# Kernel optimization log

Hardware: AMD Instinct MI355X
Metric: run time of the kernel (lower is better)

The kernel has to match this reference:

```python
import jax, jax.numpy as jnp
import numpy as np

B, N, D = 4, 256, 128
HID = 128
IN_DIM = 4 * D + 4  # h_i, h_j, |h_i-h_j|, h_i*h_j + 2 base + 2 completion feats


def setup_inputs() -> dict:
    key = jax.random.key(0)
    k1, k2, k3, k4, k5, k6, k7 = jax.random.split(key, 7)
    node_latents = jax.random.normal(k1, (B, N, D), dtype=jnp.float32)
    base_edge_logits = jax.random.normal(k2, (B, N, N), dtype=jnp.float32)
    completion_logits = jax.random.normal(k3, (B, N, N), dtype=jnp.float32)
    # MLP params (build_mlp: Linear(in,hid) -> ReLU -> Linear(hid,1) for num_layers=2)
    s1 = 1.0 / np.sqrt(IN_DIM)
    s2 = 1.0 / np.sqrt(HID)
    W1 = jax.random.uniform(k4, (IN_DIM, HID), minval=-s1, maxval=s1, dtype=jnp.float32)
    b1 = jax.random.uniform(k5, (HID,), minval=-s1, maxval=s1, dtype=jnp.float32)
    W2 = jax.random.uniform(k6, (HID, 1), minval=-s2, maxval=s2, dtype=jnp.float32)
    b2 = jax.random.uniform(k7, (1,), minval=-s2, maxval=s2, dtype=jnp.float32)
    return {"node_latents": node_latents, "base_edge_logits": base_edge_logits,
            "completion_logits": completion_logits, "W1": W1, "b1": b1, "W2": W2, "b2": b2}


def reference(node_latents, base_edge_logits, completion_logits, W1, b1, W2, b2):
    bsz, num_nodes, hidden_dim = node_latents.shape
    h_i = jnp.broadcast_to(node_latents[:, :, None, :], (bsz, num_nodes, num_nodes, hidden_dim))
    h_j = jnp.broadcast_to(node_latents[:, None, :, :], (bsz, num_nodes, num_nodes, hidden_dim))
    base = jnp.clip(base_edge_logits, -20.0, 20.0)
    comp = jnp.clip(completion_logits, -20.0, 20.0)
    pair_feat = jnp.concatenate([
        h_i, h_j, jnp.abs(h_i - h_j), h_i * h_j,
        base[..., None], jax.nn.sigmoid(base)[..., None],
        comp[..., None], jax.nn.sigmoid(comp)[..., None],
    ], axis=-1)  # [B, N, N, IN_DIM]
    hdn = jax.nn.relu(jnp.einsum('bijf,fh->bijh', pair_feat, W1) + b1)
    logits = (jnp.einsum('bijh,ho->bijo', hdn, W2) + b2)[..., 0]  # [B, N, N]
    logits = 0.5 * (logits + jnp.swapaxes(logits, 1, 2))
    diag = jnp.eye(num_nodes, dtype=bool)[None]
    return jnp.where(diag, jnp.float32(-1e9), logits)
```

## Files before the change

kernel.cpp:

```cpp
#include <hip/hip_runtime.h>
#include <cstdint>


typedef float f32x4 __attribute__((ext_vector_type(4)));

#define INV256 0.00390625f

__device__ __forceinline__ uint32_t pk4(float a, float b, float c, float d) {
  uint32_t u = __builtin_amdgcn_cvt_pk_fp8_f32(a, b, 0, false);
  u = __builtin_amdgcn_cvt_pk_fp8_f32(c, d, u, true);
  return u;
}
__device__ __forceinline__ uint32_t pkbf2(float lo, float hi) {
  uint32_t l = __builtin_bit_cast(uint32_t, lo);
  uint32_t h = __builtin_bit_cast(uint32_t, hi);
  return (l >> 16) | (h & 0xffff0000u);
}
__device__ __forceinline__ float ulo(uint32_t u) {
  return __builtin_bit_cast(float, u << 16);
}
__device__ __forceinline__ float uhi(uint32_t u) {
  return __builtin_bit_cast(float, u & 0xffff0000u);
}
__device__ __forceinline__ long mk64(uint32_t lo, uint32_t hi) {
  return (long)((((unsigned long long)hi) << 32) | lo);
}
__device__ __forceinline__ float qsum4(float v) {
  v += __builtin_bit_cast(float, __builtin_amdgcn_update_dpp(
           0, __builtin_bit_cast(int, v), 0xB1, 0xF, 0xF, true));
  v += __builtin_bit_cast(float, __builtin_amdgcn_update_dpp(
           0, __builtin_bit_cast(int, v), 0x4E, 0xF, 0xF, true));
  return v;
}

__global__ __launch_bounds__(256) void pre_k(const float* __restrict__ node,
                                             const float* __restrict__ W1,
                                             const float* __restrict__ b1,
                                             float* __restrict__ PiB,
                                             float* __restrict__ Pjf,
                                             uint32_t* __restrict__ W1f8) {
  int bid = blockIdx.x;
  int tid = threadIdx.x;
  if (bid < 32) {
    if (tid < 128) {
      int ks = bid >> 2, nip = (bid >> 1) & 1, wn = bid & 1;
      int lane = tid & 63, nilow = tid >> 6;
      int quad = lane >> 4, col = lane & 15;
      int h = wn * 64 + (nip * 2 + nilow) * 16 + col;
      int k0 = ks * 32 + quad * 8;
      float w[8];
#pragma unroll
      for (int t = 0; t < 8; ++t) w[t] = W1[(256 + k0 + t) * 128 + h] * 256.0f;
      uint2 u;
      u.x = pk4(w[0], w[1], w[2], w[3]);
      u.y = pk4(w[4], w[5], w[6], w[7]);
      reinterpret_cast<uint2*>(W1f8)[(bid * 64 + lane) * 2 + nilow] = u;
    }
    return;
  }
  __shared__ float sN[512];
  const int r0 = (bid - 32) * 4;
  {
    int d = tid & 127, rh = tid >> 7;
#pragma unroll
    for (int rr = 0; rr < 2; ++rr) {
      int row = rr * 2 + rh;
      sN[d * 4 + row] = node[(size_t)(r0 + row) * 128 + d];
    }
  }
  __syncthreads();
  const int h = tid & 127, proj = tid >> 7;
  const float* Wp = W1 + (size_t)proj * 128 * 128 + h;
  float a0 = 0.f, a1 = 0.f, a2 = 0.f, a3 = 0.f;
#pragma unroll 4
  for (int d = 0; d < 128; ++d) {
    float w = Wp[(size_t)d * 128];
    float4 v = *reinterpret_cast<const float4*>(&sN[d * 4]);
    a0 = fmaf(v.x, w, a0);
    a1 = fmaf(v.y, w, a1);
    a2 = fmaf(v.z, w, a2);
    a3 = fmaf(v.w, w, a3);
  }
  float bb = (proj == 0) ? b1[h] : 0.f;
  float* dst = (proj == 0) ? PiB : Pjf;
  dst[(size_t)(r0 + 0) * 128 + h] = 256.f * (a0 + bb);
  dst[(size_t)(r0 + 1) * 128 + h] = 256.f * (a1 + bb);
  dst[(size_t)(r0 + 2) * 128 + h] = 256.f * (a2 + bb);
  dst[(size_t)(r0 + 3) * 128 + h] = 256.f * (a3 + bb);
}

__global__ __launch_bounds__(256, 5) void main_k(
    const float* __restrict__ node, const float* __restrict__ baseL,
    const float* __restrict__ compL, const float* __restrict__ W1,
    const float* __restrict__ W2, const float* __restrict__ b2,
    const uint32_t* __restrict__ W1f8, const float* __restrict__ PiB,
    const float* __restrict__ Pjf, float* __restrict__ out) {
  __shared__ __align__(16) char smem[16384];
  __shared__ __align__(16) uint32_t sPP[16 * 132];
  __shared__ __align__(16) float sScal[64 * 12];
  char* sF = smem;
  float* sP = reinterpret_cast<float*>(smem);

  const int tid = threadIdx.x;
  const int bx = blockIdx.x;
  const int b = bx / 528;
  const int t = bx - b * 528;
  int tI = (int)((65.0f - sqrtf(4225.0f - 8.0f * (float)t)) * 0.5f);
  tI = (tI < 0) ? 0 : (tI > 31 ? 31 : tI);
  while (((65 * tI - tI * tI) >> 1) > t) --tI;
  while (tI < 31 && ((65 * (tI + 1) - (tI + 1) * (tI + 1)) >> 1) <= t) ++tI;
  const int tJ = tI + (t - ((65 * tI - tI * tI) >> 1));
  const int I0 = tI * 8, J0 = tJ * 8;
  const int rowB = b * 256;

  const int lane = tid & 63;
  const int wn2 = tid >> 6;
  const int col = lane & 15, quad = lane >> 4;

  const int uB = ((wn2 & 1) << 1) | (wn2 >> 1);
  uint4 gB[8];
#pragma unroll
  for (int ks = 0; ks < 8; ++ks)
    gB[ks] = reinterpret_cast<const uint4*>(W1f8)[(ks * 4 + uB) * 64 + lane];

#pragma unroll
  for (int it = 0; it < 2; ++it) {
    int fidx = it * 256 + tid;
    int row = fidx >> 5, d4 = fidx & 31;
    int gr = rowB + ((row < 8) ? (I0 + row) : (J0 + row - 8));
    float4 a = reinterpret_cast<const float4*>(PiB + (size_t)gr * 128)[d4];
    float4 c = reinterpret_cast<const float4*>(Pjf + (size_t)gr * 128)[d4];
    uint4 u;
    u.x = pkbf2(a.x, c.x);
    u.y = pkbf2(a.y, c.y);
    u.z = pkbf2(a.z, c.z);
    u.w = pkbf2(a.w, c.w);
    *reinterpret_cast<uint4*>(&sPP[row * 132 + d4 * 4]) = u;
  }

  if (tid < 128) {
    int p = tid & 63, dir = tid >> 6;
    int iN = I0 + (p >> 3), jN = J0 + (p & 7);
    int rr = dir ? jN : iN, cc = dir ? iN : jN;
    float bl = fminf(fmaxf(baseL[(size_t)(rowB + rr) * 256 + cc], -20.f), 20.f);
    float cl = fminf(fmaxf(compL[(size_t)(rowB + rr) * 256 + cc], -20.f), 20.f);
    float4 v;
    v.x = 256.f * bl;
    v.y = 256.f / (1.f + __expf(-bl));
    v.z = 256.f * cl;
    v.w = 256.f / (1.f + __expf(-cl));
    *reinterpret_cast<float4*>(&sScal[p * 12 + dir * 4]) = v;
  }

  float cB0[2], cB1[2], cB2[2], cB3[2], cW2[2];
#pragma unroll
  for (int ni = 0; ni < 2; ++ni) {
    int h = (wn2 * 2 + ni) * 16 + col;
    cB0[ni] = W1[512 * 128 + h];
    cB1[ni] = W1[513 * 128 + h];
    cB2[ni] = W1[514 * 128 + h];
    cB3[ni] = W1[515 * 128 + h];
    cW2[ni] = W2[h] * INV256;
  }
  const float b2v = b2[0];

  {
    const int d4 = tid & 31;
    const int rr = tid >> 5;
    const int ks1 = d4 >> 3, qd = (d4 >> 1) & 3, kb = (d4 & 1) * 4;
    const int scolbase = 2 * qd + 4 * ks1;
    const float4 hj = *reinterpret_cast<const float4*>(node + (size_t)(rowB + J0 + rr) * 128 + d4 * 4);
#pragma unroll
    for (int ii = 0; ii < 8; ++ii) {
      const float4 hi = *reinterpret_cast<const float4*>(node + (size_t)(rowB + I0 + ii) * 128 + d4 * 4);
      uint32_t du = pk4(fabsf(hi.x - hj.x), fabsf(hi.y - hj.y),
                        fabsf(hi.z - hj.z), fabsf(hi.w - hj.w));
      uint32_t pu = pk4(hi.x * hj.x, hi.y * hj.y, hi.z * hj.z, hi.w * hj.w);
      int p = ii * 8 + rr;
      int colp = p & 15, mi = p >> 4;
      int scol = (colp + scolbase) & 15;
      uint32_t addr = mi * 512 + qd * 128 + scol * 8 + kb;
      *reinterpret_cast<uint32_t*>(sF + ks1 * 2048 + addr) = du;
      *reinterpret_cast<uint32_t*>(sF + (ks1 + 4) * 2048 + addr) = pu;
    }
  }
  __syncthreads();

  f32x4 acc[4][2] = {};
#pragma unroll
  for (int ks = 0; ks < 8; ++ks) {
    long bb0 = mk64(gB[ks].x, gB[ks].y);
    long bb1 = mk64(gB[ks].z, gB[ks].w);
    const int ascol = (col + 2 * quad + 4 * (ks & 3)) & 15;
    const char* aks = sF + ks * 2048 + quad * 128 + ascol * 8;
#pragma unroll
    for (int mi = 0; mi < 4; ++mi) {
      uint2 av = *reinterpret_cast<const uint2*>(aks + mi * 512);
      long aa = mk64(av.x, av.y);
      acc[mi][0] = __builtin_amdgcn_mfma_f32_16x16x32_fp8_fp8(aa, bb0, acc[mi][0], 0, 0, 0);
      acc[mi][1] = __builtin_amdgcn_mfma_f32_16x16x32_fp8_fp8(aa, bb1, acc[mi][1], 0, 0, 0);
    }
  }
  __syncthreads();

  uint32_t uJ[4][2];
#pragma unroll
  for (int r = 0; r < 4; ++r)
#pragma unroll
    for (int ni = 0; ni < 2; ++ni)
      uJ[r][ni] = sPP[(8 + (quad & 1) * 4 + r) * 132 + (wn2 * 2 + ni) * 16 + col];

#pragma unroll
  for (int mi = 0; mi < 4; ++mi) {
    const int ii = mi * 2 + (quad >> 1);
    uint32_t uI[2];
#pragma unroll
    for (int ni = 0; ni < 2; ++ni)
      uI[ni] = sPP[ii * 132 + (wn2 * 2 + ni) * 16 + col];
#pragma unroll
    for (int r = 0; r < 4; ++r) {
      int p = mi * 16 + quad * 4 + r;
      float4 scf = *reinterpret_cast<const float4*>(&sScal[p * 12]);
      float4 scm = *reinterpret_cast<const float4*>(&sScal[p * 12 + 4]);
      float vf = 0.f, vm = 0.f;
#pragma unroll
      for (int ni = 0; ni < 2; ++ni) {
        float piI = ulo(uI[ni]), pjI = uhi(uI[ni]);
        float piJ = ulo(uJ[r][ni]), pjJ = uhi(uJ[r][ni]);
        float a = acc[mi][ni][r];
        float pf = (a + piI) + pjJ;
        pf = fmaf(scf.x, cB0[ni], pf);
        pf = fmaf(scf.y, cB1[ni], pf);
        pf = fmaf(scf.z, cB2[ni], pf);
        pf = fmaf(scf.w, cB3[ni], pf);
        float pm = (a + piJ) + pjI;
        pm = fmaf(scm.x, cB0[ni], pm);
        pm = fmaf(scm.y, cB1[ni], pm);
        pm = fmaf(scm.z, cB2[ni], pm);
        pm = fmaf(scm.w, cB3[ni], pm);
        vf = fmaf(fmaxf(pf, 0.f), cW2[ni], vf);
        vm = fmaf(fmaxf(pm, 0.f), cW2[ni], vm);
      }
      vf = qsum4(vf);
      vm = qsum4(vm);
      if ((col & 3) == 0) {
        int part = wn2 * 4 + (col >> 2);
        sP[p * 42 + part] = vf;
        sP[p * 42 + 20 + part] = vm;
      }
    }
  }
  __syncthreads();

  if (tid < 64) {
    int p = tid;
    const float2* f2 = reinterpret_cast<const float2*>(sP + p * 42);
    const float2* m2 = reinterpret_cast<const float2*>(sP + p * 42 + 20);
    float sumF = 0.f, sumM = 0.f;
#pragma unroll
    for (int c = 0; c < 8; ++c) {
      float2 a = f2[c], d = m2[c];
      sumF += a.x + a.y;
      sumM += d.x + d.y;
    }
    float val = 0.5f * (sumF + sumM) + b2v;
    int iN = I0 + (p >> 3), jN = J0 + (p & 7);
    if (iN == jN) val = -1e9f;
    out[(size_t)(rowB + iN) * 256 + jN] = val;
    out[(size_t)(rowB + jN) * 256 + iN] = val;
  }
}

extern "C" void kernel_launch(void* const* d_in, const int* in_sizes, int n_in,
                              void* d_out, int out_size, void* d_ws, size_t ws_size,
                              hipStream_t stream) {
  const float* node = (const float*)d_in[0];
  const float* baseL = (const float*)d_in[1];
  const float* compL = (const float*)d_in[2];
  const float* W1 = (const float*)d_in[3];
  const float* b1 = (const float*)d_in[4];
  const float* W2 = (const float*)d_in[5];
  const float* b2 = (const float*)d_in[6];
  float* out = (float*)d_out;

  char* ws = (char*)d_ws;
  float* PiB = (float*)(ws);
  float* Pjf = (float*)(ws + (512 << 10));
  uint32_t* W1f8 = (uint32_t*)(ws + (1024 << 10));

  pre_k<<<288, 256, 0, stream>>>(node, W1, b1, PiB, Pjf, W1f8);
  main_k<<<2112, 256, 0, stream>>>(node, baseL, compL, W1, W2, b2, W1f8, PiB, Pjf, out);
}
```

Measured before the change: 95.75 us.

## Fold per-node projection terms into MFMA via one-hot fp8 accumulation

Replaces the bf16 shared-memory staging of per-node projections (PiB/Pjf) with fp8 B-operands added into the accumulators through one-hot A-fragments in extra MFMA calls. The forward and mirrored directions are processed one after the other: the second pass subtracts the forward terms by sign-flipping the fp8 data and adds the mirrored terms. It also moves the W1 fragment loads into the MFMA loop, widens the DPP reduction to 16 lanes, shrinks shared memory, and raises the occupancy hint to 6. This cuts LDS traffic and VGPR pressure, at the cost of extra fp8 quantization error (values scaled by 1/16) and more MFMA issues.

```diff
diff --git a/kernel.cpp b/kernel.cpp
--- a/kernel.cpp
+++ b/kernel.cpp
@@ -11,26 +11,26 @@
   u = __builtin_amdgcn_cvt_pk_fp8_f32(c, d, u, true);
   return u;
 }
-__device__ __forceinline__ uint32_t pkbf2(float lo, float hi) {
-  uint32_t l = __builtin_bit_cast(uint32_t, lo);
-  uint32_t h = __builtin_bit_cast(uint32_t, hi);
-  return (l >> 16) | (h & 0xffff0000u);
-}
-__device__ __forceinline__ float ulo(uint32_t u) {
-  return __builtin_bit_cast(float, u << 16);
-}
-__device__ __forceinline__ float uhi(uint32_t u) {
-  return __builtin_bit_cast(float, u & 0xffff0000u);
-}
 __device__ __forceinline__ long mk64(uint32_t lo, uint32_t hi) {
   return (long)((((unsigned long long)hi) << 32) | lo);
 }
-__device__ __forceinline__ float qsum4(float v) {
-  v += __builtin_bit_cast(float, __builtin_amdgcn_update_dpp(
-           0, __builtin_bit_cast(int, v), 0xB1, 0xF, 0xF, true));
-  v += __builtin_bit_cast(float, __builtin_amdgcn_update_dpp(
-           0, __builtin_bit_cast(int, v), 0x4E, 0xF, 0xF, true));
+template <int CTRL>
+__device__ __forceinline__ float dppadd(float v) {
+  return v + __builtin_bit_cast(float, __builtin_amdgcn_update_dpp(
+                 0, __builtin_bit_cast(int, v), CTRL, 0xF, 0xF, true));
+}
+__device__ __forceinline__ float rowsum16(float v) {
+  v = dppadd<0xB1>(v);
+  v = dppadd<0x4E>(v);
+  v = dppadd<0x124>(v);
+  v = dppadd<0x128>(v);
   return v;
+}
+__device__ __forceinline__ uint2 onehot8(int x) {
+  uint2 u;
+  u.x = (x < 4) ? (0x58u << (x * 8)) : 0u;
+  u.y = (x >= 4) ? (0x58u << ((x - 4) * 8)) : 0u;
+  return u;
 }
 
 __global__ __launch_bounds__(256) void pre_k(const float* __restrict__ node,
@@ -89,17 +89,15 @@
   dst[(size_t)(r0 + 3) * 128 + h] = 256.f * (a3 + bb);
 }
 
-__global__ __launch_bounds__(256, 5) void main_k(
+__global__ __launch_bounds__(256, 6) void main_k(
     const float* __restrict__ node, const float* __restrict__ baseL,
     const float* __restrict__ compL, const float* __restrict__ W1,
     const float* __restrict__ W2, const float* __restrict__ b2,
     const uint32_t* __restrict__ W1f8, const float* __restrict__ PiB,
     const float* __restrict__ Pjf, float* __restrict__ out) {
-  __shared__ __align__(16) char smem[16384];
-  __shared__ __align__(16) uint32_t sPP[16 * 132];
+  __shared__ __align__(16) char sF[16384];
   __shared__ __align__(16) float sScal[64 * 12];
-  char* sF = smem;
-  float* sP = reinterpret_cast<float*>(smem);
+  __shared__ __align__(16) float sP[512];
 
   const int tid = threadIdx.x;
   const int bx = blockIdx.x;
@@ -117,25 +115,26 @@
   const int wn2 = tid >> 6;
   const int col = lane & 15, quad = lane >> 4;
 
-  const int uB = ((wn2 & 1) << 1) | (wn2 >> 1);
-  uint4 gB[8];
-#pragma unroll
-  for (int ks = 0; ks < 8; ++ks)
-    gB[ks] = reinterpret_cast<const uint4*>(W1f8)[(ks * 4 + uB) * 64 + lane];
-
-#pragma unroll
-  for (int it = 0; it < 2; ++it) {
-    int fidx = it * 256 + tid;
-    int row = fidx >> 5, d4 = fidx & 31;
-    int gr = rowB + ((row < 8) ? (I0 + row) : (J0 + row - 8));
-    float4 a = reinterpret_cast<const float4*>(PiB + (size_t)gr * 128)[d4];
-    float4 c = reinterpret_cast<const float4*>(Pjf + (size_t)gr * 128)[d4];
-    uint4 u;
-    u.x = pkbf2(a.x, c.x);
-    u.y = pkbf2(a.y, c.y);
-    u.z = pkbf2(a.z, c.z);
-    u.w = pkbf2(a.w, c.w);
-    *reinterpret_cast<uint4*>(&sPP[row * 132 + d4 * 4]) = u;
+  uint2 xBF[2] = {}, xBM[2] = {};
+  if (quad < 2) {
+    const size_t offI = (size_t)(rowB + I0) * 128;
+    const size_t offJ = (size_t)(rowB + J0) * 128;
+    const float* fA = (quad == 0) ? (PiB + offI) : (Pjf + offJ);
+    const float* mA = (quad == 0) ? (Pjf + offI) : (PiB + offJ);
+#pragma unroll
+    for (int ni = 0; ni < 2; ++ni) {
+      int h = (wn2 * 2 + ni) * 16 + col;
+      float f[8], m[8];
+#pragma unroll
+      for (int tt = 0; tt < 8; ++tt) {
+        f[tt] = fA[tt * 128 + h] * 0.0625f;
+        m[tt] = mA[tt * 128 + h] * 0.0625f;
+      }
+      xBF[ni].x = pk4(f[0], f[1], f[2], f[3]);
+      xBF[ni].y = pk4(f[4], f[5], f[6], f[7]);
+      xBM[ni].x = pk4(m[0], m[1], m[2], m[3]);
+      xBM[ni].y = pk4(m[4], m[5], m[6], m[7]);
+    }
   }
 
   if (tid < 128) {
@@ -169,10 +168,12 @@
     const int rr = tid >> 5;
     const int ks1 = d4 >> 3, qd = (d4 >> 1) & 3, kb = (d4 & 1) * 4;
     const int scolbase = 2 * qd + 4 * ks1;
-    const float4 hj = *reinterpret_cast<const float4*>(node + (size_t)(rowB + J0 + rr) * 128 + d4 * 4);
+    const float4 hj =
+        *reinterpret_cast<const float4*>(node + (size_t)(rowB + J0 + rr) * 128 + d4 * 4);
 #pragma unroll
     for (int ii = 0; ii < 8; ++ii) {
-      const float4 hi = *reinterpret_cast<const float4*>(node + (size_t)(rowB + I0 + ii) * 128 + d4 * 4);
+      const float4 hi =
+          *reinterpret_cast<const float4*>(node + (size_t)(rowB + I0 + ii) * 128 + d4 * 4);
       uint32_t du = pk4(fabsf(hi.x - hj.x), fabsf(hi.y - hj.y),
                         fabsf(hi.z - hj.z), fabsf(hi.w - hj.w));
       uint32_t pu = pk4(hi.x * hj.x, hi.y * hj.y, hi.z * hj.z, hi.w * hj.w);
@@ -186,11 +187,14 @@
   }
   __syncthreads();
 
+  const uint4* Bg = reinterpret_cast<const uint4*>(W1f8);
+  const int uB = ((wn2 & 1) << 1) | (wn2 >> 1);
   f32x4 acc[4][2] = {};
 #pragma unroll
   for (int ks = 0; ks < 8; ++ks) {
-    long bb0 = mk64(gB[ks].x, gB[ks].y);
-    long bb1 = mk64(gB[ks].z, gB[ks].w);
+    uint4 bv = Bg[(ks * 4 + uB) * 64 + lane];
+    long bb0 = mk64(bv.x, bv.y);
+    long bb1 = mk64(bv.z, bv.w);
     const int ascol = (col + 2 * quad + 4 * (ks & 3)) & 15;
     const char* aks = sF + ks * 2048 + quad * 128 + ascol * 8;
 #pragma unroll
@@ -201,73 +205,89 @@
       acc[mi][1] = __builtin_amdgcn_mfma_f32_16x16x32_fp8_fp8(aa, bb1, acc[mi][1], 0, 0, 0);
     }
   }
-  __syncthreads();
-
-  uint32_t uJ[4][2];
-#pragma unroll
-  for (int r = 0; r < 4; ++r)
-#pragma unroll
-    for (int ni = 0; ni < 2; ++ni)
-      uJ[r][ni] = sPP[(8 + (quad & 1) * 4 + r) * 132 + (wn2 * 2 + ni) * 16 + col];
-
+
+  const int jj = col & 7;
+  const uint2 axj = onehot8(jj);
+  const long xbf0 = mk64(xBF[0].x, xBF[0].y), xbf1 = mk64(xBF[1].x, xBF[1].y);
 #pragma unroll
   for (int mi = 0; mi < 4; ++mi) {
-    const int ii = mi * 2 + (quad >> 1);
-    uint32_t uI[2];
-#pragma unroll
-    for (int ni = 0; ni < 2; ++ni)
-      uI[ni] = sPP[ii * 132 + (wn2 * 2 + ni) * 16 + col];
+    uint2 axi = onehot8(mi * 2 + (col >> 3));
+    uint2 ax = (quad == 0) ? axi : ((quad == 1) ? axj : make_uint2(0u, 0u));
+    long aa = mk64(ax.x, ax.y);
+    acc[mi][0] = __builtin_amdgcn_mfma_f32_16x16x32_fp8_fp8(aa, xbf0, acc[mi][0], 0, 0, 0);
+    acc[mi][1] = __builtin_amdgcn_mfma_f32_16x16x32_fp8_fp8(aa, xbf1, acc[mi][1], 0, 0, 0);
+  }
+
+#pragma unroll
+  for (int mi = 0; mi < 4; ++mi) {
 #pragma unroll
     for (int r = 0; r < 4; ++r) {
       int p = mi * 16 + quad * 4 + r;
-      float4 scf = *reinterpret_cast<const float4*>(&sScal[p * 12]);
-      float4 scm = *reinterpret_cast<const float4*>(&sScal[p * 12 + 4]);
-      float vf = 0.f, vm = 0.f;
+      float4 sc = *reinterpret_cast<const float4*>(&sScal[p * 12]);
+      float v = 0.f;
 #pragma unroll
       for (int ni = 0; ni < 2; ++ni) {
-        float piI = ulo(uI[ni]), pjI = uhi(uI[ni]);
-        float piJ = ulo(uJ[r][ni]), pjJ = uhi(uJ[r][ni]);
-        float a = acc[mi][ni][r];
-        float pf = (a + piI) + pjJ;
-        pf = fmaf(scf.x, cB0[ni], pf);
-        pf = fmaf(scf.y, cB1[ni], pf);
-        pf = fmaf(scf.z, cB2[ni], pf);
-        pf = fmaf(scf.w, cB3[ni], pf);
-        float pm = (a + piJ) + pjI;
-        pm = fmaf(scm.x, cB0[ni], pm);
-        pm = fmaf(scm.y, cB1[ni], pm);
-        pm = fmaf(scm.z, cB2[ni], pm);
-        pm = fmaf(scm.w, cB3[ni], pm);
-        vf = fmaf(fmaxf(pf, 0.f), cW2[ni], vf);
-        vm = fmaf(fmaxf(pm, 0.f), cW2[ni], vm);
+        float pre = fmaf(sc.x, cB0[ni], acc[mi][ni][r]);
+        pre = fmaf(sc.y, cB1[ni], pre);
+        pre = fmaf(sc.z, cB2[ni], pre);
+        pre = fmaf(sc.w, cB3[ni], pre);
+        v = fmaf(fmaxf(pre, 0.f), cW2[ni], v);
       }
-      vf = qsum4(vf);
-      vm = qsum4(vm);
-      if ((col & 3) == 0) {
-        int part = wn2 * 4 + (col >> 2);
-        sP[p * 42 + part] = vf;
-        sP[p * 42 + 20 + part] = vm;
+      v = rowsum16(v);
+      if (col == 0) sP[p * 4 + wn2] = v;
+    }
+  }
+
+  const long xbf0n = mk64(xBF[0].x ^ 0x80808080u, xBF[0].y ^ 0x80808080u);
+  const long xbf1n = mk64(xBF[1].x ^ 0x80808080u, xBF[1].y ^ 0x80808080u);
+  const long xbm0 = mk64(xBM[0].x, xBM[0].y), xbm1 = mk64(xBM[1].x, xBM[1].y);
+#pragma unroll
+  for (int mi = 0; mi < 4; ++mi) {
+    uint2 axi = onehot8(mi * 2 + (col >> 3));
+    uint2 ax = (quad == 0) ? axi : ((quad == 1) ? axj : make_uint2(0u, 0u));
+    long aa = mk64(ax.x, ax.y);
+    acc[mi][0] = __builtin_amdgcn_mfma_f32_16x16x32_fp8_fp8(aa, xbf0n, acc[mi][0], 0, 0, 0);
+    acc[mi][1] = __builtin_amdgcn_mfma_f32_16x16x32_fp8_fp8(aa, xbf1n, acc[mi][1], 0, 0, 0);
+    acc[mi][0] = __builtin_amdgcn_mfma_f32_16x16x32_fp8_fp8(aa, xbm0, acc[mi][0], 0, 0, 0);
+    acc[mi][1] = __builtin_amdgcn_mfma_f32_16x16x32_fp8_fp8(aa, xbm1, acc[mi][1], 0, 0, 0);
+  }
+
+#pragma unroll
+  for (int mi = 0; mi < 4; ++mi) {
+#pragma unroll
+    for (int r = 0; r < 4; ++r) {
+      int p = mi * 16 + quad * 4 + r;
+      float4 sc = *reinterpret_cast<const float4*>(&sScal[p * 12 + 4]);
+      float v = 0.f;
+#pragma unroll
+      for (int ni = 0; ni < 2; ++ni) {
+        float pre = fmaf(sc.x, cB0[ni], acc[mi][ni][r]);
+        pre = fmaf(sc.y, cB1[ni], pre);
+        pre = fmaf(sc.z, cB2[ni], pre);
+        pre = fmaf(sc.w, cB3[ni], pre);
+        v = fmaf(fmaxf(pre, 0.f), cW2[ni], v);
       }
+      v = rowsum16(v);
+      if (col == 0) sP[256 + p * 4 + wn2] = v;
     }
   }
   __syncthreads();
 
   if (tid < 64) {
     int p = tid;
-    const float2* f2 = reinterpret_cast<const float2*>(sP + p * 42);
-    const float2* m2 = reinterpret_cast<const float2*>(sP + p * 42 + 20);
-    float sumF = 0.f, sumM = 0.f;
-#pragma unroll
-    for (int c = 0; c < 8; ++c) {
-      float2 a = f2[c], d = m2[c];
-      sumF += a.x + a.y;
-      sumM += d.x + d.y;
-    }
-    float val = 0.5f * (sumF + sumM) + b2v;
-    int iN = I0 + (p >> 3), jN = J0 + (p & 7);
-    if (iN == jN) val = -1e9f;
-    out[(size_t)(rowB + iN) * 256 + jN] = val;
-    out[(size_t)(rowB + jN) * 256 + iN] = val;
+    int pii = p >> 3, pjj = p & 7;
+    if (!(tI == tJ && pii > pjj)) {
+      float4 f4 = *reinterpret_cast<const float4*>(&sP[p * 4]);
+      float4 m4 = *reinterpret_cast<const float4*>(&sP[256 + p * 4]);
+      float val = 0.5f * ((f4.x + f4.y + f4.z + f4.w) + (m4.x + m4.y + m4.z + m4.w)) + b2v;
+      int iN = I0 + pii, jN = J0 + pjj;
+      if (iN == jN) {
+        out[(size_t)(rowB + iN) * 256 + jN] = -1e9f;
+      } else {
+        out[(size_t)(rowB + iN) * 256 + jN] = val;
+        out[(size_t)(rowB + jN) * 256 + iN] = val;
+      }
+    }
   }
 }
 
```

New measurement: 111.0 us. 15.9% more time.
